# Optimization experiments

Measured on AMD Instinct MI355X. Metric: run time of the kernel, lower is better.

## Reference

```python
import jax, jax.numpy as jnp
import numpy as np

N_NODES = 5000
N_EDGES = 50000
HIDDEN = 64
EDGE_DIM = 16


def setup_inputs() -> dict:
    key = jax.random.key(0)
    ks = jax.random.split(key, 8)
    d = HIDDEN
    h = jax.random.normal(ks[0], (N_NODES, d), dtype=jnp.float32)
    edge_index = jax.random.randint(ks[1], (2, N_EDGES), 0, N_NODES, dtype=jnp.int64)
    edge_features = jax.random.normal(ks[2], (N_EDGES, EDGE_DIM), dtype=jnp.float32)
    # edge-network MLP: Linear(edge_dim, d) -> ReLU -> Linear(d, d*d)
    W1 = jax.random.normal(ks[3], (EDGE_DIM, d), dtype=jnp.float32) * (1.0 / np.sqrt(EDGE_DIM))
    b1 = jnp.zeros((d,), dtype=jnp.float32)
    W2 = jax.random.normal(ks[4], (d, d * d), dtype=jnp.float32) * (1.0 / np.sqrt(d))
    b2 = jnp.zeros((d * d,), dtype=jnp.float32)
    # GRUCell params (torch layout: rows = [reset; update; new])
    W_ih = jax.random.normal(ks[5], (3 * d, d), dtype=jnp.float32) * (1.0 / np.sqrt(d))
    W_hh = jax.random.normal(ks[6], (3 * d, d), dtype=jnp.float32) * (1.0 / np.sqrt(d))
    b_ih = jnp.zeros((3 * d,), dtype=jnp.float32)
    b_hh = jnp.zeros((3 * d,), dtype=jnp.float32)
    return {"h": h, "edge_index": edge_index, "edge_features": edge_features,
            "W1": W1, "b1": b1, "W2": W2, "b2": b2,
            "W_ih": W_ih, "W_hh": W_hh, "b_ih": b_ih, "b_hh": b_hh}


def reference(h, edge_index, edge_features, W1, b1, W2, b2, W_ih, W_hh, b_ih, b_hh):
    n_nodes, d = h.shape
    src, tgt = edge_index[0], edge_index[1]
    # 1) gather sender states
    h_w = h[src]  # (E, d)
    # 2-3) edge MLP -> per-edge transformation matrices (E, d, d)
    A = jax.nn.relu(edge_features @ W1 + b1) @ W2 + b2
    A = A.reshape(-1, d, d)
    # 4) per-edge matvec messages
    msg = jnp.einsum('eij,ej->ei', A, h_w)  # (E, d)
    # 5) scatter-sum aggregation per target node
    m = jax.ops.segment_sum(msg, tgt, num_segments=n_nodes)  # (N, d)
    # 6) GRUCell(m, h) - torch semantics
    gi = m @ W_ih.T + b_ih   # (N, 3d)
    gh = h @ W_hh.T + b_hh   # (N, 3d)
    i_r, i_z, i_n = jnp.split(gi, 3, axis=-1)
    h_r, h_z, h_n = jnp.split(gh, 3, axis=-1)
    r = jax.nn.sigmoid(i_r + h_r)
    z = jax.nn.sigmoid(i_z + h_z)
    n = jnp.tanh(i_n + r * h_n)
    h_new = (1.0 - z) * n + z * h
    return h_new
```

## Files before the change

kernel.cpp:

```cpp
#include <hip/hip_runtime.h>
#include <math.h>

#define N_NODES 5000
#define N_EDGES 50000
#define NPAD 5024
#define KP 4224
#define POISON_I ((int)0xAAAAAAAAu)

typedef _Float16 f16x8 __attribute__((ext_vector_type(8)));
typedef _Float16 f16x2 __attribute__((ext_vector_type(2)));
typedef float    f32x4 __attribute__((ext_vector_type(4)));

static __device__ __forceinline__ f32x4 mfma16f(f16x8 a, f16x8 b, f32x4 c) {
    return __builtin_amdgcn_mfma_f32_16x16x32_f16(a, b, c, 0, 0, 0);
}

__global__ void prep_kernel(const float* __restrict__ W2, const float* __restrict__ b2,
                            const float* __restrict__ Wih, const float* __restrict__ Whh,
                            const int* __restrict__ ei,
                            _Float16* __restrict__ Br, _Float16* __restrict__ Bg2,
                            int* __restrict__ cnt) {
    int g = blockIdx.x * 256 + threadIdx.x;
    if (g < 33792) {
        int nt = g / 8448, rem = g - nt * 8448;
        int ks = rem >> 6, lane = rem & 63;
        int lo = lane & 15, q = lane >> 4;
        int i = nt * 16 + lo, kap0 = ks * 32 + q * 8;
        f16x8 v;
#pragma unroll
        for (int p = 0; p < 8; ++p) {
            int kap = kap0 + p;
            int k2 = kap >> 7, rem2 = kap & 127;
            int j = rem2 >> 1, k = k2 * 2 + (rem2 & 1);
            float x = 0.f;
            if (k < 64) x = W2[(size_t)k * 4096 + i * 64 + j];
            else if (k == 64) x = b2[i * 64 + j];
            v[p] = (_Float16)x;
        }
        *(f16x8*)(Br + (size_t)g * 8) = v;
        return;
    }
    g -= 33792;
    if (g < 3072) {
        int ct = g >> 7, ks = (g >> 6) & 1, lane = g & 63;
        int lo = lane & 15, q = lane >> 4;
        const float* src = (ct < 12) ? Wih : Whh;
        int r = ((ct < 12) ? ct : ct - 12) * 16 + lo;
        int j0 = ks * 32 + q * 8;
        f16x8 v;
#pragma unroll
        for (int p = 0; p < 8; ++p) v[p] = (_Float16)src[r * 64 + j0 + p];
        *(f16x8*)(Bg2 + (size_t)g * 8) = v;
        return;
    }
    g -= 3072;
    if (g < N_EDGES) atomicAdd(&cnt[ei[N_EDGES + g]], 1);
}

__global__ __launch_bounds__(1024) void scan_kernel(const int* __restrict__ cnt,
                                                    int* __restrict__ off,
                                                    int* __restrict__ cur) {
    __shared__ int s[1024];
    int tid = threadIdx.x;
    int base = tid * 5;
    int loc[5]; int sum = 0;
#pragma unroll
    for (int q = 0; q < 5; ++q) {
        int v = (base + q < N_NODES) ? (cnt[base + q] - POISON_I) : 0;
        loc[q] = sum; sum += v;
    }
    s[tid] = sum; __syncthreads();
    for (int d = 1; d < 1024; d <<= 1) {
        int v = (tid >= d) ? s[tid - d] : 0;
        __syncthreads();
        s[tid] += v;
        __syncthreads();
    }
    int excl = (tid > 0) ? s[tid - 1] : 0;
#pragma unroll
    for (int q = 0; q < 5; ++q)
        if (base + q < N_NODES) { off[base + q] = excl + loc[q]; cur[base + q] = excl + loc[q]; }
    if (tid == 1023) off[N_NODES] = excl + sum;
}

__global__ void scatter_kernel(const int* __restrict__ ei, int* __restrict__ cur,
                               int* __restrict__ srcp, int* __restrict__ eidp) {
    int e = blockIdx.x * 256 + threadIdx.x;
    if (e < N_EDGES) {
        int q = atomicAdd(&cur[ei[N_EDGES + e]], 1);
        srcp[q] = ei[e];
        eidp[q] = e;
    }
}

__global__ __launch_bounds__(256) void hbuild_kernel(const int* __restrict__ toff,
                                                     const int* __restrict__ srcp,
                                                     const int* __restrict__ eidp,
                                                     const float* __restrict__ ef,
                                                     const float* __restrict__ W1,
                                                     const float* __restrict__ b1,
                                                     const float* __restrict__ h,
                                                     _Float16* __restrict__ H) {
    __shared__ _Float16 tls[16][64];
    __shared__ float hls[16][64];
    int tid = threadIdx.x, kc = tid >> 6, lane = tid & 63;
    int v = blockIdx.x;
    float acc[16];
#pragma unroll
    for (int k = 0; k < 16; ++k) acc[k] = 0.f;
    float acc64 = 0.f;
    int s0 = 0, s1 = 0;
    if (v < N_NODES) { s0 = toff[v]; s1 = toff[v + 1]; }
    float w1c[16];
#pragma unroll
    for (int k = 0; k < 16; ++k) w1c[k] = W1[k * 64 + lane];
    float b1l = b1[lane];
    for (int tb = s0; tb < s1; tb += 16) {
        int tcnt = s1 - tb; if (tcnt > 16) tcnt = 16;
        int eidx[4], sidx[4];
#pragma unroll
        for (int r = 0; r < 4; ++r) {
            int idx = kc * 4 + r;
            if (idx < tcnt) {
                eidx[r] = eidp[tb + idx];
                sidx[r] = srcp[tb + idx];
            }
        }
#pragma unroll
        for (int r = 0; r < 4; ++r) {
            int idx = kc * 4 + r;
            if (idx < tcnt) {
                hls[idx][lane] = h[(size_t)sidx[r] * 64 + lane];
                const float* efr = ef + (size_t)eidx[r] * 16;
                float tacc = b1l;
#pragma unroll
                for (int k = 0; k < 16; ++k) tacc += efr[k] * w1c[k];
                tls[idx][lane] = (_Float16)fmaxf(tacc, 0.f);
            }
        }
        __syncthreads();
        int q = 0;
        for (; q + 1 < tcnt; q += 2) {
            float hv0 = hls[q][lane];
            float hv1 = hls[q + 1][lane];
            const f16x8* t0 = (const f16x8*)&tls[q][kc * 16];
            const f16x8* t1 = (const f16x8*)&tls[q + 1][kc * 16];
            f16x8 a0 = t0[0], a1 = t0[1];
            f16x8 c0 = t1[0], c1 = t1[1];
#pragma unroll
            for (int p = 0; p < 8; ++p) {
                acc[p]     += (float)a0[p] * hv0 + (float)c0[p] * hv1;
                acc[8 + p] += (float)a1[p] * hv0 + (float)c1[p] * hv1;
            }
            acc64 += hv0 + hv1;
        }
        if (q < tcnt) {
            float hv = hls[q][lane];
            const f16x8* t0 = (const f16x8*)&tls[q][kc * 16];
            f16x8 a0 = t0[0], a1 = t0[1];
#pragma unroll
            for (int p = 0; p < 8; ++p) {
                acc[p]     += (float)a0[p] * hv;
                acc[8 + p] += (float)a1[p] * hv;
            }
            acc64 += hv;
        }
        __syncthreads();
    }
    _Float16* Hv = H + (size_t)v * KP;
#pragma unroll
    for (int p = 0; p < 8; ++p) {
        f16x2 pv = { (_Float16)acc[p * 2], (_Float16)acc[p * 2 + 1] };
        *(f16x2*)(Hv + (kc * 8 + p) * 128 + lane * 2) = pv;
    }
    if (kc == 3) {
        f16x2 pv = { (_Float16)acc64, (_Float16)0.f };
        *(f16x2*)(Hv + 32 * 128 + lane * 2) = pv;
    }
}

__global__ __launch_bounds__(512) void gemm_gru(const _Float16* __restrict__ H,
                                                const _Float16* __restrict__ Br,
                                                const _Float16* __restrict__ Bg2,
                                                const float* __restrict__ h,
                                                const float* __restrict__ bih,
                                                const float* __restrict__ bhh,
                                                float* __restrict__ out) {
    __shared__ _Float16 As[2][16 * 136];
    __shared__ float    mbuf[16][65];
    __shared__ _Float16 mls[16 * 72];
    __shared__ _Float16 hls[16 * 72];
    __shared__ float    gbuf[16 * 385];
    int tid = threadIdx.x, w8 = tid >> 6, lane = tid & 63;
    int lo = lane & 15, q = lane >> 4;
    int nt = w8 & 3, kh = w8 >> 2;
    int m0 = blockIdx.x * 16;
    int ar = tid >> 4, ac = (tid & 15) * 8;
    const _Float16* Ag = H + (size_t)(m0 + ar) * KP + ac;
    const f16x8* BrV = (const f16x8*)Br;
    f32x4 acc = {0.f, 0.f, 0.f, 0.f};
    if (tid < 256)
        *(f16x8*)(&As[0][ar * 136 + ac]) = *(const f16x8*)(Ag);
    f16x8 b0 = BrV[((size_t)(nt * 132 + kh * 2 + 0)) * 64 + lane];
    f16x8 b1 = BrV[((size_t)(nt * 132 + kh * 2 + 1)) * 64 + lane];
    __syncthreads();
    for (int c = 0; c < 33; ++c) {
        f16x8 pf, nb0, nb1;
        if (tid < 256 && c + 1 < 33)
            pf = *(const f16x8*)(Ag + (size_t)(c + 1) * 128);
        if (c + 1 < 33) {
            nb0 = BrV[((size_t)(nt * 132 + (c + 1) * 4 + kh * 2 + 0)) * 64 + lane];
            nb1 = BrV[((size_t)(nt * 132 + (c + 1) * 4 + kh * 2 + 1)) * 64 + lane];
        }
        const _Float16* Ab = &As[c & 1][0];
        f16x8 a0 = *(const f16x8*)(Ab + lo * 136 + (kh * 2 + 0) * 32 + q * 8);
        f16x8 a1 = *(const f16x8*)(Ab + lo * 136 + (kh * 2 + 1) * 32 + q * 8);
        acc = mfma16f(a0, b0, acc);
        acc = mfma16f(a1, b1, acc);
        if (tid < 256 && c + 1 < 33)
            *(f16x8*)(&As[(c + 1) & 1][ar * 136 + ac]) = pf;
        __syncthreads();
        b0 = nb0; b1 = nb1;
    }
    if (kh == 1) {
#pragma unroll
        for (int g = 0; g < 4; ++g) mbuf[q * 4 + g][nt * 16 + lo] = acc[g];
    }
    __syncthreads();
    if (kh == 0) {
#pragma unroll
        for (int g = 0; g < 4; ++g) {
            float mv = acc[g] + mbuf[q * 4 + g][nt * 16 + lo];
            mls[(q * 4 + g) * 72 + nt * 16 + lo] = (_Float16)mv;
        }
    } else {
        int t2 = (w8 - 4) * 64 + lane;
#pragma unroll
        for (int r = 0; r < 4; ++r) {
            int e = r * 256 + t2, nl = e >> 6, j = e & 63;
            int n = m0 + nl;
            float hv = (n < N_NODES) ? h[(size_t)n * 64 + j] : 0.f;
            hls[nl * 72 + j] = (_Float16)hv;
        }
    }
    __syncthreads();
    f16x8 am0 = *(const f16x8*)&mls[lo * 72 + q * 8];
    f16x8 am1 = *(const f16x8*)&mls[lo * 72 + 32 + q * 8];
    f16x8 ah0 = *(const f16x8*)&hls[lo * 72 + q * 8];
    f16x8 ah1 = *(const f16x8*)&hls[lo * 72 + 32 + q * 8];
    const f16x8* BgV = (const f16x8*)Bg2;
    f32x4 z4 = {0.f, 0.f, 0.f, 0.f};
    f32x4 ga[3] = {z4, z4, z4};
#pragma unroll
    for (int j = 0; j < 3; ++j) {
        int ct = w8 + 8 * j;
        f16x8 bg0 = BgV[((size_t)(ct * 2 + 0)) * 64 + lane];
        f16x8 bg1 = BgV[((size_t)(ct * 2 + 1)) * 64 + lane];
        f16x8 a0f = (ct < 12) ? am0 : ah0;
        f16x8 a1f = (ct < 12) ? am1 : ah1;
        ga[j] = mfma16f(a0f, bg0, ga[j]);
        ga[j] = mfma16f(a1f, bg1, ga[j]);
    }
#pragma unroll
    for (int j = 0; j < 3; ++j) {
        int ct = w8 + 8 * j;
        int col = (ct < 12) ? (ct * 16 + lo) : (192 + (ct - 12) * 16 + lo);
#pragma unroll
        for (int g = 0; g < 4; ++g) gbuf[(q * 4 + g) * 385 + col] = ga[j][g];
    }
    __syncthreads();
    int i = lane;
#pragma unroll
    for (int u = 0; u < 2; ++u) {
        int nl = w8 * 2 + u, n = m0 + nl;
        if (n >= N_NODES) continue;
        const float* gb = gbuf + nl * 385;
        float ir  = gb[i]       + bih[i];
        float iz  = gb[64 + i]  + bih[64 + i];
        float inn = gb[128 + i] + bih[128 + i];
        float hr  = gb[192 + i] + bhh[i];
        float hz  = gb[256 + i] + bhh[64 + i];
        float hn  = gb[320 + i] + bhh[128 + i];
        float hval = h[(size_t)n * 64 + i];
        float r = 1.f / (1.f + expf(-(ir + hr)));
        float z = 1.f / (1.f + expf(-(iz + hz)));
        float nn = tanhf(inn + r * hn);
        out[n * 64 + i] = (1.f - z) * nn + z * hval;
    }
}

extern "C" void kernel_launch(void* const* d_in, const int* in_sizes, int n_in,
                              void* d_out, int out_size, void* d_ws, size_t ws_size,
                              hipStream_t stream) {
    const float* h   = (const float*)d_in[0];
    const int*   ei  = (const int*)d_in[1];
    const float* ef  = (const float*)d_in[2];
    const float* W1  = (const float*)d_in[3];
    const float* b1  = (const float*)d_in[4];
    const float* W2  = (const float*)d_in[5];
    const float* b2  = (const float*)d_in[6];
    const float* Wih = (const float*)d_in[7];
    const float* Whh = (const float*)d_in[8];
    const float* bih = (const float*)d_in[9];
    const float* bhh = (const float*)d_in[10];
    float* out = (float*)d_out;

    _Float16* H    = (_Float16*)d_ws;
    _Float16* Br   = H + (size_t)NPAD * KP;
    _Float16* Bg2  = Br + 270336;
    int*      cnt  = (int*)(Bg2 + 24576);
    int*      toff = cnt + N_NODES;
    int*      cur  = toff + N_NODES + 1;
    int*      srcp = cur + N_NODES;
    int*      eidp = srcp + N_EDGES;

    prep_kernel<<<340, 256, 0, stream>>>(W2, b2, Wih, Whh, ei, Br, Bg2, cnt);
    scan_kernel<<<1, 1024, 0, stream>>>(cnt, toff, cur);
    scatter_kernel<<<196, 256, 0, stream>>>(ei, cur, srcp, eidp);
    hbuild_kernel<<<NPAD, 256, 0, stream>>>(toff, srcp, eidp, ef, W1, b1, h, H);
    gemm_gru<<<314, 512, 0, stream>>>(H, Br, Bg2, h, bih, bhh, out);
}
```

Measured before the change: 135.8 us.

## Fuse per-node outer-product build into the GEMM+GRU kernel via shared memory

Replaces the separate hbuild kernel, which wrote a large per-node fp16 H matrix (N x 4224) to global memory, with a single fused kernel. Each 16-node block computes edge MLP hidden activations and gathered sender states into shared memory in batches, forms the outer-product accumulators in registers per K chunk, stages them in LDS, and feeds them directly into MFMA against the reshaped W2 before the GRU stage. This removes the H write/read round trip and one launch. In exchange, only 313 blocks run and the edge batch loop is repeated four times, so parallelism drops and the edge preprocessing work is duplicated.

Result: slower. 190.2 us (+40.1%).

```diff
diff --git a/kernel.cpp b/kernel.cpp
--- a/kernel.cpp
+++ b/kernel.cpp
@@ -3,11 +3,11 @@
 
 #define N_NODES 5000
 #define N_EDGES 50000
-#define NPAD 5024
-#define KP 4224
+#define EB 96
 #define POISON_I ((int)0xAAAAAAAAu)
 
 typedef _Float16 f16x8 __attribute__((ext_vector_type(8)));
+typedef _Float16 f16x4 __attribute__((ext_vector_type(4)));
 typedef _Float16 f16x2 __attribute__((ext_vector_type(2)));
 typedef float    f32x4 __attribute__((ext_vector_type(4)));
 
@@ -93,144 +93,143 @@
     }
 }
 
-__global__ __launch_bounds__(256) void hbuild_kernel(const int* __restrict__ toff,
-                                                     const int* __restrict__ srcp,
-                                                     const int* __restrict__ eidp,
-                                                     const float* __restrict__ ef,
-                                                     const float* __restrict__ W1,
-                                                     const float* __restrict__ b1,
-                                                     const float* __restrict__ h,
-                                                     _Float16* __restrict__ H) {
-    __shared__ _Float16 tls[16][64];
-    __shared__ float hls[16][64];
-    int tid = threadIdx.x, kc = tid >> 6, lane = tid & 63;
-    int v = blockIdx.x;
-    float acc[16];
-#pragma unroll
-    for (int k = 0; k < 16; ++k) acc[k] = 0.f;
-    float acc64 = 0.f;
-    int s0 = 0, s1 = 0;
-    if (v < N_NODES) { s0 = toff[v]; s1 = toff[v + 1]; }
-    float w1c[16];
-#pragma unroll
-    for (int k = 0; k < 16; ++k) w1c[k] = W1[k * 64 + lane];
-    float b1l = b1[lane];
-    for (int tb = s0; tb < s1; tb += 16) {
-        int tcnt = s1 - tb; if (tcnt > 16) tcnt = 16;
-        int eidx[4], sidx[4];
-#pragma unroll
-        for (int r = 0; r < 4; ++r) {
-            int idx = kc * 4 + r;
-            if (idx < tcnt) {
-                eidx[r] = eidp[tb + idx];
-                sidx[r] = srcp[tb + idx];
-            }
-        }
-#pragma unroll
-        for (int r = 0; r < 4; ++r) {
-            int idx = kc * 4 + r;
-            if (idx < tcnt) {
-                hls[idx][lane] = h[(size_t)sidx[r] * 64 + lane];
-                const float* efr = ef + (size_t)eidx[r] * 16;
-                float tacc = b1l;
-#pragma unroll
-                for (int k = 0; k < 16; ++k) tacc += efr[k] * w1c[k];
-                tls[idx][lane] = (_Float16)fmaxf(tacc, 0.f);
-            }
-        }
-        __syncthreads();
-        int q = 0;
-        for (; q + 1 < tcnt; q += 2) {
-            float hv0 = hls[q][lane];
-            float hv1 = hls[q + 1][lane];
-            const f16x8* t0 = (const f16x8*)&tls[q][kc * 16];
-            const f16x8* t1 = (const f16x8*)&tls[q + 1][kc * 16];
-            f16x8 a0 = t0[0], a1 = t0[1];
-            f16x8 c0 = t1[0], c1 = t1[1];
-#pragma unroll
-            for (int p = 0; p < 8; ++p) {
-                acc[p]     += (float)a0[p] * hv0 + (float)c0[p] * hv1;
-                acc[8 + p] += (float)a1[p] * hv0 + (float)c1[p] * hv1;
-            }
-            acc64 += hv0 + hv1;
-        }
-        if (q < tcnt) {
-            float hv = hls[q][lane];
-            const f16x8* t0 = (const f16x8*)&tls[q][kc * 16];
-            f16x8 a0 = t0[0], a1 = t0[1];
-#pragma unroll
-            for (int p = 0; p < 8; ++p) {
-                acc[p]     += (float)a0[p] * hv;
-                acc[8 + p] += (float)a1[p] * hv;
-            }
-            acc64 += hv;
-        }
-        __syncthreads();
-    }
-    _Float16* Hv = H + (size_t)v * KP;
-#pragma unroll
-    for (int p = 0; p < 8; ++p) {
-        f16x2 pv = { (_Float16)acc[p * 2], (_Float16)acc[p * 2 + 1] };
-        *(f16x2*)(Hv + (kc * 8 + p) * 128 + lane * 2) = pv;
-    }
-    if (kc == 3) {
-        f16x2 pv = { (_Float16)acc64, (_Float16)0.f };
-        *(f16x2*)(Hv + 32 * 128 + lane * 2) = pv;
-    }
-}
-
-__global__ __launch_bounds__(512) void gemm_gru(const _Float16* __restrict__ H,
-                                                const _Float16* __restrict__ Br,
-                                                const _Float16* __restrict__ Bg2,
-                                                const float* __restrict__ h,
-                                                const float* __restrict__ bih,
-                                                const float* __restrict__ bhh,
-                                                float* __restrict__ out) {
-    __shared__ _Float16 As[2][16 * 136];
-    __shared__ float    mbuf[16][65];
-    __shared__ _Float16 mls[16 * 72];
-    __shared__ _Float16 hls[16 * 72];
-    __shared__ float    gbuf[16 * 385];
+__global__ __launch_bounds__(512, 4) void fused_gnn(
+    const int* __restrict__ toff, const int* __restrict__ srcp,
+    const int* __restrict__ eidp, const float* __restrict__ ef,
+    const float* __restrict__ W1, const float* __restrict__ b1,
+    const float* __restrict__ h, const _Float16* __restrict__ Br,
+    const _Float16* __restrict__ Bg2, const float* __restrict__ bih,
+    const float* __restrict__ bhh, float* __restrict__ out)
+{
+    __shared__ __align__(16) char smem[69888];
+    _Float16* As  = (_Float16*)(smem);
+    _Float16* tfh = (_Float16*)(smem + 33024);
+    float*    hfs = (float*)(smem + 45312);
+    float*    gbuf  = (float*)(smem);
+    _Float16* mls   = (_Float16*)(smem + 24640);
+    _Float16* hls16 = (_Float16*)(smem + 26944);
+    float*    mbuf  = (float*)(smem + 29248);
+
     int tid = threadIdx.x, w8 = tid >> 6, lane = tid & 63;
     int lo = lane & 15, q = lane >> 4;
     int nt = w8 & 3, kh = w8 >> 2;
+    int g32 = tid >> 5, t32 = tid & 31;
+    int k2loc = t32 >> 2, jb = t32 & 3;
     int m0 = blockIdx.x * 16;
-    int ar = tid >> 4, ac = (tid & 15) * 8;
-    const _Float16* Ag = H + (size_t)(m0 + ar) * KP + ac;
+
+    int E0 = toff[m0];
+    int mhi = m0 + 16; if (mhi > N_NODES) mhi = N_NODES;
+    int etot = toff[mhi] - E0;
+    int na = m0 + g32;     if (na > N_NODES) na = N_NODES;
+    int nb = m0 + g32 + 1; if (nb > N_NODES) nb = N_NODES;
+    int ns0 = toff[na] - E0, ns1 = toff[nb] - E0;
+
+    float w1c[16];
+#pragma unroll
+    for (int k = 0; k < 16; ++k) w1c[k] = W1[k * 64 + lane];
+    float b1l = b1[lane];
+
     const f16x8* BrV = (const f16x8*)Br;
-    f32x4 acc = {0.f, 0.f, 0.f, 0.f};
-    if (tid < 256)
-        *(f16x8*)(&As[0][ar * 136 + ac]) = *(const f16x8*)(Ag);
-    f16x8 b0 = BrV[((size_t)(nt * 132 + kh * 2 + 0)) * 64 + lane];
-    f16x8 b1 = BrV[((size_t)(nt * 132 + kh * 2 + 1)) * 64 + lane];
-    __syncthreads();
-    for (int c = 0; c < 33; ++c) {
-        f16x8 pf, nb0, nb1;
-        if (tid < 256 && c + 1 < 33)
-            pf = *(const f16x8*)(Ag + (size_t)(c + 1) * 128);
-        if (c + 1 < 33) {
-            nb0 = BrV[((size_t)(nt * 132 + (c + 1) * 4 + kh * 2 + 0)) * 64 + lane];
-            nb1 = BrV[((size_t)(nt * 132 + (c + 1) * 4 + kh * 2 + 1)) * 64 + lane];
-        }
-        const _Float16* Ab = &As[c & 1][0];
-        f16x8 a0 = *(const f16x8*)(Ab + lo * 136 + (kh * 2 + 0) * 32 + q * 8);
-        f16x8 a1 = *(const f16x8*)(Ab + lo * 136 + (kh * 2 + 1) * 32 + q * 8);
-        acc = mfma16f(a0, b0, acc);
-        acc = mfma16f(a1, b1, acc);
-        if (tid < 256 && c + 1 < 33)
-            *(f16x8*)(&As[(c + 1) & 1][ar * 136 + ac]) = pf;
+    f32x4 macc0 = {0.f, 0.f, 0.f, 0.f}, macc1 = macc0;
+    float sacc0 = 0.f, sacc1 = 0.f;
+    int nbat = (etot + EB - 1) / EB;
+
+    for (int kc = 0; kc < 4; ++kc) {
+        float gacc[32];
+#pragma unroll
+        for (int i = 0; i < 32; ++i) gacc[i] = 0.f;
+        for (int b = 0; b < nbat; ++b) {
+            int ebase = b * EB;
+            int bcnt = etot - ebase; if (bcnt > EB) bcnt = EB;
+            __syncthreads();
+            for (int r = 0; r < EB / 8; ++r) {
+                int eloc = r * 8 + w8;
+                if (eloc < bcnt) {
+                    int ge = E0 + ebase + eloc;
+                    int src = srcp[ge], eid = eidp[ge];
+                    hfs[eloc * 64 + lane] = h[(size_t)src * 64 + lane];
+                    const float* efr = ef + (size_t)eid * 16;
+                    float tacc = b1l;
+#pragma unroll
+                    for (int k = 0; k < 16; ++k) tacc += efr[k] * w1c[k];
+                    tfh[eloc * 64 + lane] = (_Float16)fmaxf(tacc, 0.f);
+                }
+            }
+            __syncthreads();
+            int e0 = ns0 - ebase; if (e0 < 0) e0 = 0;
+            int e1 = ns1 - ebase; if (e1 > bcnt) e1 = bcnt;
+            for (int e = e0; e < e1; ++e) {
+                f16x2 tp = *(const f16x2*)&tfh[e * 64 + kc * 16 + k2loc * 2];
+                float t0f = (float)tp[0], t1f = (float)tp[1];
+                const f32x4* hr4 = (const f32x4*)&hfs[e * 64 + jb * 16];
+#pragma unroll
+                for (int v4 = 0; v4 < 4; ++v4) {
+                    f32x4 hv = hr4[v4];
+#pragma unroll
+                    for (int jj = 0; jj < 4; ++jj) {
+                        gacc[(v4 * 4 + jj) * 2 + 0] += t0f * hv[jj];
+                        gacc[(v4 * 4 + jj) * 2 + 1] += t1f * hv[jj];
+                    }
+                }
+            }
+            if (kc == 0) {
+                for (int e = e0; e < e1; ++e) {
+                    sacc0 += hfs[e * 64 + t32 * 2];
+                    sacc1 += hfs[e * 64 + t32 * 2 + 1];
+                }
+            }
+        }
         __syncthreads();
-        b0 = nb0; b1 = nb1;
-    }
+        {
+            _Float16* aw = As + g32 * 1032 + k2loc * 128 + jb * 32;
+#pragma unroll
+            for (int bq = 0; bq < 4; ++bq) {
+                f16x8 wv;
+#pragma unroll
+                for (int p = 0; p < 8; ++p) wv[p] = (_Float16)gacc[bq * 8 + p];
+                *(f16x8*)(aw + bq * 8) = wv;
+            }
+        }
+        __syncthreads();
+        const _Float16* Arow = As + lo * 1032 + q * 8;
+#pragma unroll
+        for (int s = 0; s < 8; ++s) {
+            int ksl = kh * 16 + s * 2;
+            f16x8 a0 = *(const f16x8*)(Arow + ksl * 32);
+            f16x8 a1 = *(const f16x8*)(Arow + (ksl + 1) * 32);
+            f16x8 b0 = BrV[(size_t)(nt * 132 + kc * 32 + ksl) * 64 + lane];
+            f16x8 b1v = BrV[(size_t)(nt * 132 + kc * 32 + ksl + 1) * 64 + lane];
+            macc0 = mfma16f(a0, b0, macc0);
+            macc1 = mfma16f(a1, b1v, macc1);
+        }
+    }
+    __syncthreads();
+    {
+        f16x4 tw = { (_Float16)sacc0, (_Float16)0.f, (_Float16)sacc1, (_Float16)0.f };
+        *(f16x4*)(As + g32 * 1032 + t32 * 4) = tw;
+    }
+    __syncthreads();
+    {
+        const _Float16* Arow = As + lo * 1032 + q * 8;
+        int ksl = kh * 2;
+        f16x8 a0 = *(const f16x8*)(Arow + ksl * 32);
+        f16x8 a1 = *(const f16x8*)(Arow + (ksl + 1) * 32);
+        f16x8 b0 = BrV[(size_t)(nt * 132 + 128 + ksl) * 64 + lane];
+        f16x8 b1v = BrV[(size_t)(nt * 132 + 128 + ksl + 1) * 64 + lane];
+        macc0 = mfma16f(a0, b0, macc0);
+        macc1 = mfma16f(a1, b1v, macc1);
+    }
+    f32x4 macc = macc0 + macc1;
+    __syncthreads();
     if (kh == 1) {
 #pragma unroll
-        for (int g = 0; g < 4; ++g) mbuf[q * 4 + g][nt * 16 + lo] = acc[g];
+        for (int g = 0; g < 4; ++g) mbuf[(q * 4 + g) * 65 + nt * 16 + lo] = macc[g];
     }
     __syncthreads();
     if (kh == 0) {
 #pragma unroll
         for (int g = 0; g < 4; ++g) {
-            float mv = acc[g] + mbuf[q * 4 + g][nt * 16 + lo];
+            float mv = macc[g] + mbuf[(q * 4 + g) * 65 + nt * 16 + lo];
             mls[(q * 4 + g) * 72 + nt * 16 + lo] = (_Float16)mv;
         }
     } else {
@@ -240,22 +239,22 @@
             int e = r * 256 + t2, nl = e >> 6, j = e & 63;
             int n = m0 + nl;
             float hv = (n < N_NODES) ? h[(size_t)n * 64 + j] : 0.f;
-            hls[nl * 72 + j] = (_Float16)hv;
+            hls16[nl * 72 + j] = (_Float16)hv;
         }
     }
     __syncthreads();
     f16x8 am0 = *(const f16x8*)&mls[lo * 72 + q * 8];
     f16x8 am1 = *(const f16x8*)&mls[lo * 72 + 32 + q * 8];
-    f16x8 ah0 = *(const f16x8*)&hls[lo * 72 + q * 8];
-    f16x8 ah1 = *(const f16x8*)&hls[lo * 72 + 32 + q * 8];
+    f16x8 ah0 = *(const f16x8*)&hls16[lo * 72 + q * 8];
+    f16x8 ah1 = *(const f16x8*)&hls16[lo * 72 + 32 + q * 8];
     const f16x8* BgV = (const f16x8*)Bg2;
     f32x4 z4 = {0.f, 0.f, 0.f, 0.f};
     f32x4 ga[3] = {z4, z4, z4};
 #pragma unroll
     for (int j = 0; j < 3; ++j) {
         int ct = w8 + 8 * j;
-        f16x8 bg0 = BgV[((size_t)(ct * 2 + 0)) * 64 + lane];
-        f16x8 bg1 = BgV[((size_t)(ct * 2 + 1)) * 64 + lane];
+        f16x8 bg0 = BgV[(size_t)(ct * 2 + 0) * 64 + lane];
+        f16x8 bg1 = BgV[(size_t)(ct * 2 + 1) * 64 + lane];
         f16x8 a0f = (ct < 12) ? am0 : ah0;
         f16x8 a1f = (ct < 12) ? am1 : ah1;
         ga[j] = mfma16f(a0f, bg0, ga[j]);
@@ -305,8 +304,7 @@
     const float* bhh = (const float*)d_in[10];
     float* out = (float*)d_out;
 
-    _Float16* H    = (_Float16*)d_ws;
-    _Float16* Br   = H + (size_t)NPAD * KP;
+    _Float16* Br   = (_Float16*)d_ws;
     _Float16* Bg2  = Br + 270336;
     int*      cnt  = (int*)(Bg2 + 24576);
     int*      toff = cnt + N_NODES;
@@ -317,6 +315,6 @@
     prep_kernel<<<340, 256, 0, stream>>>(W2, b2, Wih, Whh, ei, Br, Bg2, cnt);
     scan_kernel<<<1, 1024, 0, stream>>>(cnt, toff, cur);
     scatter_kernel<<<196, 256, 0, stream>>>(ei, cur, srcp, eidp);
-    hbuild_kernel<<<NPAD, 256, 0, stream>>>(toff, srcp, eidp, ef, W1, b1, h, H);
-    gemm_gru<<<314, 512, 0, stream>>>(H, Br, Bg2, h, bih, bhh, out);
-}
+    fused_gnn<<<313, 512, 0, stream>>>(toff, srcp, eidp, ef, W1, b1, h,
+                                       Br, Bg2, bih, bhh, out);
+}
```
